# Optimization experiments

Measured on AMD Instinct MI355X. Metric: run time of the kernel, lower is better.

Reference implementation:

```python
import jax, jax.numpy as jnp
import numpy as np

N = 10000        # nodes
F_IN = 128       # node features (data.num_node_features)
OUT = 16         # out_channels
H = 32           # attention heads
C1 = 4 * OUT     # hidden per-head dim (4*out_channels)
E = 80000        # directed edges
EPS = 1e-5       # BatchNorm eps
NEG = 0.2        # GATConv LeakyReLU negative_slope


def _gat(x, src, dst, W, a_s, a_d, b, n, C):
    # PyG GATConv, shared lin, concat=False (mean over heads)
    h = (x @ W).reshape(n, H, C)                    # [n,H,C]
    e_src = jnp.sum(h * a_s, -1)                    # [n,H] (alpha from x_j)
    e_dst = jnp.sum(h * a_d, -1)                    # [n,H] (alpha from x_i)
    e = jax.nn.leaky_relu(e_src[src] + e_dst[dst], NEG)     # [E',H]
    m = jax.ops.segment_max(e, dst, num_segments=n)         # segment softmax
    p = jnp.exp(e - m[dst])
    z = jax.ops.segment_sum(p, dst, num_segments=n)
    alpha = p / z[dst]
    out = jax.ops.segment_sum(alpha[:, :, None] * h[src], dst, num_segments=n)
    return out.mean(1) + b                          # mean over heads + bias


def _bn(x, g, b, m, v):  # eval-mode BatchNorm1d (running stats)
    return (x - m) * g / jnp.sqrt(v + EPS) + b


def setup_inputs():
    k = jax.random.split(jax.random.key(0), 40)
    rn = lambda i, s, sc=0.1: jax.random.normal(k[i], s, jnp.float32) * sc
    d = {"x": jax.random.normal(k[0], (N, F_IN), jnp.float32),
         "edge_index": jax.random.randint(k[1], (2, E), 0, N, jnp.int32)}
    # 4 GATConv layers
    d.update(W1=rn(2, (F_IN, H * C1)), as1=rn(3, (H, C1)), ad1=rn(4, (H, C1)), b1=rn(5, (C1,)))
    d.update(W2=rn(6, (C1, H * OUT)), as2=rn(7, (H, OUT)), ad2=rn(8, (H, OUT)), b2=rn(9, (OUT,)))
    d.update(W3=rn(10, (F_IN, H * C1)), as3=rn(11, (H, C1)), ad3=rn(12, (H, C1)), b3=rn(13, (C1,)))
    d.update(W4=rn(14, (C1, H * OUT)), as4=rn(15, (H, OUT)), ad4=rn(16, (H, OUT)), b4=rn(17, (OUT,)))
    # ResidualNetwork(1 block): 1x1 Conv1d over L=1 == matmul
    d.update(rwa=rn(18, (F_IN, OUT)), rba=rn(19, (OUT,)),
             bn1g=jnp.ones(OUT), bn1b=jnp.zeros(OUT), bn1m=rn(20, (OUT,)), bn1v=jnp.abs(rn(21, (OUT,))) + 1.0,
             rwb=rn(22, (OUT, OUT)), rbb=rn(23, (OUT,)),
             bn2g=jnp.ones(OUT), bn2b=jnp.zeros(OUT), bn2m=rn(24, (OUT,)), bn2v=jnp.abs(rn(25, (OUT,))) + 1.0,
             wsc=rn(26, (F_IN, OUT)), bsc=rn(27, (OUT,)),
             bnsg=jnp.ones(OUT), bnsb=jnp.zeros(OUT), bnsm=rn(28, (OUT,)), bnsv=jnp.abs(rn(29, (OUT,))) + 1.0,
             wfc=rn(30, (OUT, OUT)), bfc=rn(31, (OUT,)))
    return d


def reference(x, edge_index, W1, as1, ad1, b1, W2, as2, ad2, b2,
              W3, as3, ad3, b3, W4, as4, ad4, b4,
              rwa, rba, bn1g, bn1b, bn1m, bn1v, rwb, rbb, bn2g, bn2b, bn2m, bn2v,
              wsc, bsc, bnsg, bnsb, bnsm, bnsv, wfc, bfc):
    n = x.shape[0]
    loops = jnp.arange(n, dtype=edge_index.dtype)  # add_self_loops=True
    s2t_src = jnp.concatenate([edge_index[0], loops])  # flow source_to_target
    s2t_dst = jnp.concatenate([edge_index[1], loops])
    t2s_src = jnp.concatenate([edge_index[1], loops])  # flow target_to_source
    t2s_dst = jnp.concatenate([edge_index[0], loops])
    # dropout in original is unassigned (no-op); eval mode assumed
    x_s = jax.nn.elu(_gat(x, s2t_src, s2t_dst, W1, as1, ad1, b1, n, C1))
    x_in = jax.nn.elu(_gat(x_s, s2t_src, s2t_dst, W2, as2, ad2, b2, n, OUT))
    x_t = jax.nn.elu(_gat(x, t2s_src, t2s_dst, W3, as3, ad3, b3, n, C1))
    x_out = jax.nn.elu(_gat(x_t, t2s_src, t2s_dst, W4, as4, ad4, b4, n, OUT))
    # ResidualNetwork: block + identity avg-pool (L=1) + fc
    h = jax.nn.relu(_bn(x @ rwa + rba, bn1g, bn1b, bn1m, bn1v))
    h = _bn(h @ rwb + rbb, bn2g, bn2b, bn2m, bn2v)
    sc = _bn(x @ wsc + bsc, bnsg, bnsb, bnsm, bnsv)
    x_self = jax.nn.relu(h + sc) @ wfc + bfc
    return (x_in, x_out, x_self)
```

## Files before the change

kernel.cpp:

```cpp
#include <hip/hip_runtime.h>
#include <stdint.h>

__device__ __forceinline__ float bf2f(unsigned short u) {
  union { unsigned int i; float f; } v; v.i = ((unsigned int)u) << 16; return v.f;
}
__device__ __forceinline__ unsigned short f2bf(float f) {
  union { float f; unsigned int i; } v; v.f = f;
  unsigned int i = v.i;
  unsigned int r = (i + 0x7fffu + ((i >> 16) & 1u)) >> 16;
  return (unsigned short)r;
}

typedef __bf16 bf16x8 __attribute__((ext_vector_type(8)));
typedef float f32x4 __attribute__((ext_vector_type(4)));
union ABfrag { int4 i4; bf16x8 v; };

#if __has_builtin(__builtin_amdgcn_cvt_pk_fp8_f32) && __has_builtin(__builtin_amdgcn_cvt_pk_f32_fp8)
#define HW_FP8 1
#else
#define HW_FP8 0
#endif

__device__ __forceinline__ unsigned char f2fp8_sw(float f) {
  union { float f; unsigned int u; } v; v.f = f;
  unsigned int s = (v.u >> 24) & 0x80;
  float a = fabsf(f);
  if (a >= 448.f) return (unsigned char)(s | 0x7E);
  v.f = a;
  int ex = (int)(v.u >> 23);
  unsigned int man = v.u & 0x7FFFFFu;
  if (ex >= 121) {
    unsigned int val = ((unsigned int)(ex - 120) << 3) | (man >> 20);
    unsigned int rem = man & 0xFFFFFu;
    if (rem > 0x80000u || (rem == 0x80000u && (val & 1))) val++;
    if (val > 0x7E) val = 0x7E;
    return (unsigned char)(s | val);
  }
  int q = (int)(a * 512.f + 0.5f);
  if (q > 8) q = 8;
  return (unsigned char)(s | (unsigned int)q);
}
__device__ __forceinline__ float fp8dec_sw(unsigned char c) {
  unsigned int e = (c >> 3) & 15u, m = c & 7u;
  float v;
  if (e) { union { unsigned int u; float f; } x; x.u = ((e + 120) << 23) | (m << 20); v = x.f; }
  else v = (float)m * 0.001953125f;
  return (c & 0x80) ? -v : v;
}
__device__ __forceinline__ unsigned char f2fp8(float f) {
#if HW_FP8
  int v = __builtin_amdgcn_cvt_pk_fp8_f32(f, f, 0, false);
  return (unsigned char)(v & 0xFF);
#else
  return f2fp8_sw(f);
#endif
}
__device__ __forceinline__ void dec16(int4 g, float o[16]) {
#if HW_FP8
  { auto p = __builtin_amdgcn_cvt_pk_f32_fp8(g.x, false); o[0]=p[0]; o[1]=p[1]; }
  { auto p = __builtin_amdgcn_cvt_pk_f32_fp8(g.x, true ); o[2]=p[0]; o[3]=p[1]; }
  { auto p = __builtin_amdgcn_cvt_pk_f32_fp8(g.y, false); o[4]=p[0]; o[5]=p[1]; }
  { auto p = __builtin_amdgcn_cvt_pk_f32_fp8(g.y, true ); o[6]=p[0]; o[7]=p[1]; }
  { auto p = __builtin_amdgcn_cvt_pk_f32_fp8(g.z, false); o[8]=p[0]; o[9]=p[1]; }
  { auto p = __builtin_amdgcn_cvt_pk_f32_fp8(g.z, true ); o[10]=p[0]; o[11]=p[1]; }
  { auto p = __builtin_amdgcn_cvt_pk_f32_fp8(g.w, false); o[12]=p[0]; o[13]=p[1]; }
  { auto p = __builtin_amdgcn_cvt_pk_f32_fp8(g.w, true ); o[14]=p[0]; o[15]=p[1]; }
#else
  unsigned int w[4] = {(unsigned)g.x, (unsigned)g.y, (unsigned)g.z, (unsigned)g.w};
#pragma unroll
  for (int d = 0; d < 4; ++d)
#pragma unroll
    for (int b = 0; b < 4; ++b) o[d*4+b] = fp8dec_sw((unsigned char)((w[d] >> (b*8)) & 0xFF));
#endif
}

__global__ __launch_bounds__(256) void k_detect(const unsigned int* __restrict__ x, int* flag) {
  __shared__ int cnt;
  if (threadIdx.x == 0) cnt = 0;
  __syncthreads();
  int c = 0;
  for (int i = threadIdx.x; i < 1024; i += 256) {
    unsigned int lo = x[i] & 0xFFFFu;
    int ex = (int)((lo >> 7) & 0xFF);
    if (ex >= 100 && ex <= 140) c++;
  }
  atomicAdd(&cnt, c);
  __syncthreads();
  if (threadIdx.x == 0) flag[0] = (cnt > 600) ? 1 : 0;
}

struct PrepDesc {
  const void* csrc[32]; float* cdst[32]; int cn[32];
  const void* x; float* xc; unsigned short* xp;
  const void* W1; const void* W2; const void* W3; const void* W4;
  unsigned short* P1; unsigned short* P2; unsigned short* P3; unsigned short* P4;
  int* degAB;
  int nxb;
  int xtotal;
  int ctotal;
  int ndeg2;
};
__global__ __launch_bounds__(256) void k_prep(PrepDesc d, const int* __restrict__ flag) {
  int isbf = *flag;
  int b = blockIdx.x;
  if (b < d.nxb) {
    int i = b * 256 + threadIdx.x;
    if (i < d.xtotal) {
      float v = isbf ? bf2f(((const unsigned short*)d.x)[i]) : ((const float*)d.x)[i];
      d.xc[i] = v;
      int row = i >> 7, c = i & 127;
      int tm = row >> 4, mr = row & 15;
      int s = c >> 5, quad = (c >> 3) & 3, j = c & 7;
      size_t idx = (((size_t)tm * 4 + s) * 64 + quad * 16 + mr) * 8 + j;
      d.xp[idx] = f2bf(v);
    }
    return;
  }
  b -= d.nxb;
  if (b < 288) {
    int u = b * 256 + threadIdx.x;
    const void* W; unsigned short* P; int K, N, lu;
    if (u < 32768)      { W = d.W1; P = d.P1; K = 128; N = 2048; lu = u; }
    else if (u < 36864) { W = d.W2; P = d.P2; K = 64;  N = 512;  lu = u - 32768; }
    else if (u < 69632) { W = d.W3; P = d.P3; K = 128; N = 2048; lu = u - 36864; }
    else                { W = d.W4; P = d.P4; K = 64;  N = 512;  lu = u - 69632; }
    int ksteps = K >> 5;
    int g = lu / (ksteps * 64);
    int rem = lu - g * (ksteps * 64);
    int s = rem >> 6, lane = rem & 63;
    int mr = lane & 15, quad = lane >> 4;
    int col = g * 16 + mr;
    int kbase = s * 32 + quad * 8;
#pragma unroll
    for (int j = 0; j < 8; ++j) {
      size_t src = (size_t)(kbase + j) * N + col;
      float v = isbf ? bf2f(((const unsigned short*)W)[src]) : ((const float*)W)[src];
      P[(size_t)lu * 8 + j] = f2bf(v);
    }
    return;
  }
  b -= 288;
  if (b < 4) {
    for (int idx = b * 256 + threadIdx.x; idx < d.ctotal; idx += 4 * 256) {
      int t = 0, off = idx;
      while (off >= d.cn[t]) { off -= d.cn[t]; ++t; }
      float v = isbf ? bf2f(((const unsigned short*)d.csrc[t])[off])
                     : ((const float*)d.csrc[t])[off];
      d.cdst[t][off] = v;
    }
    return;
  }
  b -= 4;
  for (int idx = b * 256 + threadIdx.x; idx < d.ndeg2; idx += 8 * 256) d.degAB[idx] = 0;
}

__global__ __launch_bounds__(256) void k_deg_count(const int* __restrict__ ei, int* degA, int* degB, int E) {
  int e = blockIdx.x * 256 + threadIdx.x;
  if (e < E) { atomicAdd(&degA[ei[E + e]], 1); atomicAdd(&degB[ei[e]], 1); }
}
__global__ __launch_bounds__(1024) void k_exscan2(const int* __restrict__ degA, const int* __restrict__ degB,
                                                  int* __restrict__ rowA, int* __restrict__ rowB,
                                                  int* __restrict__ colA, int* __restrict__ colB,
                                                  int* __restrict__ curA, int* __restrict__ curB, int n) {
  const int* deg = (blockIdx.x == 0) ? degA : degB;
  int* row = (blockIdx.x == 0) ? rowA : rowB;
  int* colx = (blockIdx.x == 0) ? colA : colB;
  int* curx = (blockIdx.x == 0) ? curA : curB;
  __shared__ int wsum[16], wbase[16];
  __shared__ int carry;
  if (threadIdx.x == 0) carry = 0;
  __syncthreads();
  int lane = threadIdx.x & 63, w = threadIdx.x >> 6;
  int chunks = (n + 1023) >> 10;
  for (int ch = 0; ch < chunks; ++ch) {
    int i = (ch << 10) + threadIdx.x;
    int v = (i < n) ? deg[i] : 0;
    int sc = v;
#pragma unroll
    for (int o = 1; o < 64; o <<= 1) { int t = __shfl_up(sc, o); if (lane >= o) sc += t; }
    if (lane == 63) wsum[w] = sc;
    __syncthreads();
    if (threadIdx.x < 16) {
      int v2 = wsum[threadIdx.x], s2 = v2;
#pragma unroll
      for (int o = 1; o < 16; o <<= 1) { int t = __shfl_up(s2, o); if (lane >= o) s2 += t; }
      wbase[threadIdx.x] = s2 - v2;
      if (threadIdx.x == 15) wsum[15] = s2;
    }
    __syncthreads();
    if (i < n) {
      int rv = carry + wbase[w] + (sc - v) + i;
      row[i] = rv;
      colx[rv] = i;
      curx[i] = rv + 1;
    }
    __syncthreads();
    if (threadIdx.x == 0) carry += wsum[15];
    __syncthreads();
  }
  if (threadIdx.x == 0) row[n] = carry + n;
}
__global__ __launch_bounds__(256) void k_scatter(const int* __restrict__ ei, int* colA, int* colB,
                                                 int* curA, int* curB, int E) {
  int e = blockIdx.x * 256 + threadIdx.x;
  if (e < E) {
    int s = ei[e], d = ei[E + e];
    colA[atomicAdd(&curA[d], 1)] = s;
    colB[atomicAdd(&curB[s], 1)] = d;
  }
}

template<int CH, int KSTEPS>
__global__ __launch_bounds__(256) void k_mm_es(const unsigned short* __restrict__ Ap,
                                               const unsigned short* __restrict__ Bp,
                                               unsigned char* __restrict__ C,
                                               const float* __restrict__ a_s,
                                               const float* __restrict__ a_d,
                                               float* __restrict__ es, float* __restrict__ ed,
                                               int M, int N) {
  __shared__ unsigned char tile[4][16][64];
  int wid = threadIdx.x >> 6;
  int wg = blockIdx.x * 4 + wid;
  int ntiles = N >> 6;
  int tm = wg / ntiles, tn = wg % ntiles;
  int lane = threadIdx.x & 63;
  int mr = lane & 15, quad = lane >> 4;
  const unsigned short* ap = Ap + ((size_t)tm * KSTEPS) * 512 + lane * 8;
  const unsigned short* bp = Bp + ((size_t)tn * 4 * KSTEPS) * 512 + lane * 8;
  f32x4 acc[4];
#pragma unroll
  for (int i = 0; i < 4; i++) acc[i] = (f32x4){0.f, 0.f, 0.f, 0.f};
#pragma unroll
  for (int s = 0; s < KSTEPS; ++s) {
    ABfrag a; a.i4 = *(const int4*)(ap + s * 512);
#pragma unroll
    for (int nt = 0; nt < 4; ++nt) {
      ABfrag b; b.i4 = *(const int4*)(bp + (size_t)(nt * KSTEPS + s) * 512);
      acc[nt] = __builtin_amdgcn_mfma_f32_16x16x32_bf16(a.v, b.v, acc[nt], 0, 0, 0);
    }
  }
#pragma unroll
  for (int nt = 0; nt < 4; ++nt)
#pragma unroll
    for (int r = 0; r < 4; ++r)
      tile[wid][quad * 4 + r][nt * 16 + mr] = f2fp8(acc[nt][r]);
  __syncthreads();
  {
    int r16 = lane >> 2, seg = lane & 3;
    int4 val = *(const int4*)&tile[wid][r16][seg * 16];
    *(int4*)(C + (size_t)(tm * 16 + r16) * N + tn * 64 + seg * 16) = val;
  }
  if (CH == 64) {
    float pes[4] = {0.f,0.f,0.f,0.f}, ped[4] = {0.f,0.f,0.f,0.f};
    const float* asr = a_s + tn * 64;
    const float* adr = a_d + tn * 64;
#pragma unroll
    for (int nt = 0; nt < 4; ++nt) {
      float ws = asr[nt * 16 + mr], wd = adr[nt * 16 + mr];
#pragma unroll
      for (int r = 0; r < 4; ++r) { pes[r] += acc[nt][r] * ws; ped[r] += acc[nt][r] * wd; }
    }
#pragma unroll
    for (int m = 1; m < 16; m <<= 1)
#pragma unroll
      for (int r = 0; r < 4; ++r) {
        pes[r] += __shfl_xor(pes[r], m);
        ped[r] += __shfl_xor(ped[r], m);
      }
    if (mr == 0) {
#pragma unroll
      for (int r = 0; r < 4; ++r) {
        int row = tm * 16 + quad * 4 + r;
        es[row * 32 + tn] = pes[r];
        ed[row * 32 + tn] = ped[r];
      }
    }
  } else {
    float pes[4][4], ped[4][4];
#pragma unroll
    for (int nt = 0; nt < 4; ++nt) {
      float ws = a_s[(tn * 4 + nt) * 16 + mr];
      float wd = a_d[(tn * 4 + nt) * 16 + mr];
#pragma unroll
      for (int r = 0; r < 4; ++r) { pes[nt][r] = acc[nt][r] * ws; ped[nt][r] = acc[nt][r] * wd; }
    }
#pragma unroll
    for (int m = 1; m < 16; m <<= 1)
#pragma unroll
      for (int nt = 0; nt < 4; ++nt)
#pragma unroll
        for (int r = 0; r < 4; ++r) {
          pes[nt][r] += __shfl_xor(pes[nt][r], m);
          ped[nt][r] += __shfl_xor(ped[nt][r], m);
        }
    if (mr == 0) {
#pragma unroll
      for (int nt = 0; nt < 4; ++nt)
#pragma unroll
        for (int r = 0; r < 4; ++r) {
          int row = tm * 16 + quad * 4 + r;
          es[row * 32 + tn * 4 + nt] = pes[nt][r];
          ed[row * 32 + tn * 4 + nt] = ped[nt][r];
        }
    }
  }
}

__device__ __forceinline__ float lrelu_clamp(float e) {
  e = (e > 0.f) ? e : 0.2f * e;
  return fminf(e, 80.f);
}

__global__ __launch_bounds__(256) void k_gather64(const unsigned char* __restrict__ h,
                                                  const float* __restrict__ es, const float* __restrict__ ed,
                                                  const int* __restrict__ rowp, const int* __restrict__ col,
                                                  const float* __restrict__ bias,
                                                  unsigned short* __restrict__ outp, int n) {
  int wid = threadIdx.x >> 6, lane = threadIdx.x & 63;
  int i = blockIdx.x * 4 + wid;
  if (i >= n) return;
  int hd0 = lane >> 2, hd1 = 16 + hd0;
  float e0 = ed[i * 32 + hd0];
  float e1 = ed[i * 32 + hd1];
  int beg = rowp[i], end = rowp[i + 1];
  int deg = end - beg;
  int colv = (lane < deg) ? col[beg + lane] : 0;
  float acc0[16], acc1[16];
#pragma unroll
  for (int k = 0; k < 16; ++k) { acc0[k] = 0.f; acc1[k] = 0.f; }
  float Z0 = 0.f, Z1 = 0.f;
  for (int j = 0; j < deg; ++j) {
    int s = (j < 64) ? __shfl(colv, j) : col[beg + j];
    const int4* hp = (const int4*)(h + (size_t)s * 2048);
    int4 g0 = hp[lane];
    int4 g1 = hp[64 + lane];
    float q0 = __expf(lrelu_clamp(es[s * 32 + hd0] + e0));
    float q1 = __expf(lrelu_clamp(es[s * 32 + hd1] + e1));
    Z0 += q0; Z1 += q1;
    float d0[16], d1[16];
    dec16(g0, d0); dec16(g1, d1);
#pragma unroll
    for (int k = 0; k < 16; ++k) { acc0[k] += q0 * d0[k]; acc1[k] += q1 * d1[k]; }
  }
  float zi0 = 1.0f / Z0, zi1 = 1.0f / Z1;
  float v[16];
#pragma unroll
  for (int k = 0; k < 16; ++k) v[k] = acc0[k] * zi0 + acc1[k] * zi1;
#pragma unroll
  for (int m = 4; m < 64; m <<= 1)
#pragma unroll
    for (int k = 0; k < 16; ++k) v[k] += __shfl_xor(v[k], m);
  if (lane < 4) {
    int tm = i >> 4, mr = i & 15;
    unsigned short ob[16];
#pragma unroll
    for (int k = 0; k < 16; ++k) {
      float t = v[k] * (1.f / 32.f) + bias[lane * 16 + k];
      t = (t > 0.f) ? t : (__expf(t) - 1.f);
      ob[k] = f2bf(t);
    }
    int s0 = lane >> 1;
#pragma unroll
    for (int g2 = 0; g2 < 2; ++g2) {
      size_t idx = (((size_t)tm * 2 + s0) * 64 + ((lane & 1) * 2 + g2) * 16 + mr) * 8;
      *(int4*)(outp + idx) = *(const int4*)(ob + g2 * 8);
    }
  }
}

__global__ __launch_bounds__(256) void k_gather16(const unsigned char* __restrict__ h,
                                                  const float* __restrict__ es, const float* __restrict__ ed,
                                                  const int* __restrict__ rowp, const int* __restrict__ col,
                                                  const float* __restrict__ bias,
                                                  void* __restrict__ outbase, size_t elem_off, int n,
                                                  const int* __restrict__ flag) {
  int wid = threadIdx.x >> 6, lane = threadIdx.x & 63;
  int i = blockIdx.x * 4 + wid;
  if (i >= n) return;
  int hh = lane & 31, j2 = lane >> 5;
  float ev = ed[i * 32 + hh];
  int beg = rowp[i], end = rowp[i + 1];
  int deg = end - beg;
  int colv = (lane < deg) ? col[beg + lane] : 0;
  float acc[16];
#pragma unroll
  for (int k = 0; k < 16; ++k) acc[k] = 0.f;
  float Z = 0.f;
  for (int j = j2; j < deg; j += 2) {
    int s = (j < 64) ? __shfl(colv, j) : col[beg + j];
    int4 g = ((const int4*)(h + (size_t)s * 512))[hh];
    float q = __expf(lrelu_clamp(es[s * 32 + hh] + ev));
    Z += q;
    float d[16];
    dec16(g, d);
#pragma unroll
    for (int k = 0; k < 16; ++k) acc[k] += q * d[k];
  }
  Z += __shfl_xor(Z, 32);
  float zi = 1.0f / Z;
  float v[16];
#pragma unroll
  for (int k = 0; k < 16; ++k) v[k] = acc[k] * zi;
#pragma unroll
  for (int m = 1; m < 64; m <<= 1)
#pragma unroll
    for (int k = 0; k < 16; ++k) v[k] += __shfl_xor(v[k], m);
  if (lane == 0) {
    int isbf = *flag;
    if (isbf) {
      unsigned short ob[16];
#pragma unroll
      for (int k = 0; k < 16; ++k) {
        float t = v[k] * (1.f / 32.f) + bias[k];
        t = (t > 0.f) ? t : (__expf(t) - 1.f);
        ob[k] = f2bf(t);
      }
      unsigned short* o = (unsigned short*)outbase + elem_off + (size_t)i * 16;
      *(int4*)o = *(const int4*)ob;
      *(int4*)(o + 8) = *(const int4*)(ob + 8);
    } else {
      float* o = (float*)outbase + elem_off + (size_t)i * 16;
#pragma unroll
      for (int k = 0; k < 16; ++k) {
        float t = v[k] * (1.f / 32.f) + bias[k];
        t = (t > 0.f) ? t : (__expf(t) - 1.f);
        o[k] = t;
      }
    }
  }
}

__global__ __launch_bounds__(256) void k_residual(const float* __restrict__ x,
    const float* __restrict__ rwa, const float* __restrict__ rba,
    const float* __restrict__ bn1g, const float* __restrict__ bn1b,
    const float* __restrict__ bn1m, const float* __restrict__ bn1v,
    const float* __restrict__ rwb, const float* __restrict__ rbb,
    const float* __restrict__ bn2g, const float* __restrict__ bn2b,
    const float* __restrict__ bn2m, const float* __restrict__ bn2v,
    const float* __restrict__ wsc, const float* __restrict__ bsc,
    const float* __restrict__ bnsg, const float* __restrict__ bnsb,
    const float* __restrict__ bnsm, const float* __restrict__ bnsv,
    const float* __restrict__ wfc, const float* __restrict__ bfc,
    void* __restrict__ outbase, size_t elem_off, int n, const int* __restrict__ flag) {
  __shared__ float xs[16][128];
  __shared__ float ha[16][16];
  __shared__ float tt[16][16];
  int nodebase = blockIdx.x * 16;
  for (int t = threadIdx.x; t < 16 * 128; t += 256)
    xs[t >> 7][t & 127] = x[(size_t)(nodebase + (t >> 7)) * 128 + (t & 127)];
  __syncthreads();
  int ni = threadIdx.x >> 4, c = threadIdx.x & 15;
  float ya = 0.f, ysc = 0.f;
  for (int k = 0; k < 128; ++k) {
    float xv = xs[ni][k];
    ya  += xv * rwa[k * 16 + c];
    ysc += xv * wsc[k * 16 + c];
  }
  ya += rba[c]; ysc += bsc[c];
  float s1 = bn1g[c] * rsqrtf(bn1v[c] + 1e-5f);
  ya = (ya - bn1m[c]) * s1 + bn1b[c];
  ya = fmaxf(ya, 0.f);
  float ss = bnsg[c] * rsqrtf(bnsv[c] + 1e-5f);
  ysc = (ysc - bnsm[c]) * ss + bnsb[c];
  ha[ni][c] = ya;
  __syncthreads();
  float h2 = rbb[c];
  for (int k = 0; k < 16; ++k) h2 += ha[ni][k] * rwb[k * 16 + c];
  float s2 = bn2g[c] * rsqrtf(bn2v[c] + 1e-5f);
  h2 = (h2 - bn2m[c]) * s2 + bn2b[c];
  tt[ni][c] = fmaxf(h2 + ysc, 0.f);
  __syncthreads();
  float o = bfc[c];
  for (int k = 0; k < 16; ++k) o += tt[ni][k] * wfc[k * 16 + c];
  size_t oo = elem_off + (size_t)(nodebase + ni) * 16 + c;
  if (*flag) ((unsigned short*)outbase)[oo] = f2bf(o);
  else       ((float*)outbase)[oo] = o;
}

extern "C" void kernel_launch(void* const* d_in, const int* in_sizes, int n_in,
                              void* d_out, int out_size, void* d_ws, size_t ws_size,
                              hipStream_t stream) {
  const int n = in_sizes[0] / 128;
  const int E = in_sizes[1] / 2;
  const int* ei = (const int*)d_in[1];

  char* wsp = (char*)d_ws; size_t off = 0;
  auto alloc = [&](size_t bytes) -> void* {
    void* p = wsp + off; off = (off + bytes + 255) & ~(size_t)255; return p;
  };
  int* flag = (int*)alloc(4);
  float* xc = (float*)alloc((size_t)n * 128 * 4);
  unsigned short* xp = (unsigned short*)alloc((size_t)n * 128 * 2);
  unsigned short* W1p = (unsigned short*)alloc((size_t)2048 * 128 * 2);
  unsigned short* W2p = (unsigned short*)alloc((size_t)512 * 64 * 2);
  unsigned short* W3p = (unsigned short*)alloc((size_t)2048 * 128 * 2);
  unsigned short* W4p = (unsigned short*)alloc((size_t)512 * 64 * 2);
  unsigned char* hbuf = (unsigned char*)alloc((size_t)n * 2048);
  unsigned char* hbuf2 = hbuf;
  float* es = (float*)alloc((size_t)n * 32 * 4);
  float* ed = (float*)alloc((size_t)n * 32 * 4);
  unsigned short* xsp = (unsigned short*)alloc((size_t)n * 64 * 2);
  unsigned short* xtp = (unsigned short*)alloc((size_t)n * 64 * 2);
  int* rowA = (int*)alloc((size_t)(n + 1) * 4);
  int* rowB = (int*)alloc((size_t)(n + 1) * 4);
  int* colA = (int*)alloc((size_t)(E + n) * 4);
  int* colB = (int*)alloc((size_t)(E + n) * 4);
  int* degAB = (int*)alloc((size_t)2 * n * 4);
  int* degA = degAB, * degB = degAB + n;
  int* curA = (int*)alloc((size_t)n * 4);
  int* curB = (int*)alloc((size_t)n * 4);

  static const int cidx[32] = {3,4,5, 7,8,9, 11,12,13, 15,16,17,
                               18,19,20,21,22,23,24,25,26,27,28,29,
                               30,31,32,33,34,35,36,37};
  PrepDesc pd;
  float* canon[38] = {nullptr};
  pd.ctotal = 0;
  for (int t = 0; t < 32; ++t) {
    int ii = cidx[t];
    canon[ii] = (float*)alloc((size_t)in_sizes[ii] * 4);
    pd.csrc[t] = d_in[ii];
    pd.cdst[t] = canon[ii];
    pd.cn[t] = in_sizes[ii];
    pd.ctotal += in_sizes[ii];
  }
  pd.x = d_in[0]; pd.xc = xc; pd.xp = xp;
  pd.W1 = d_in[2]; pd.W2 = d_in[6]; pd.W3 = d_in[10]; pd.W4 = d_in[14];
  pd.P1 = W1p; pd.P2 = W2p; pd.P3 = W3p; pd.P4 = W4p;
  pd.degAB = degAB;
  pd.nxb = (n * 128 + 255) / 256;
  pd.xtotal = n * 128;
  pd.ndeg2 = 2 * n;
  (void)ws_size; (void)n_in; (void)out_size;

  k_detect<<<1, 256, 0, stream>>>((const unsigned int*)d_in[0], flag);
  k_prep<<<pd.nxb + 288 + 4 + 8, 256, 0, stream>>>(pd, flag);

  k_deg_count<<<(E + 255) / 256, 256, 0, stream>>>(ei, degA, degB, E);
  k_exscan2<<<2, 1024, 0, stream>>>(degA, degB, rowA, rowB, colA, colB, curA, curB, n);
  k_scatter<<<(E + 255) / 256, 256, 0, stream>>>(ei, colA, colB, curA, curB, E);

  const int mt = n / 16;
  const int gb = (n + 3) / 4;
  k_mm_es<64,4><<<mt * 32 / 4, 256, 0, stream>>>(xp, W1p, hbuf, canon[3], canon[4], es, ed, n, 2048);
  k_gather64<<<gb, 256, 0, stream>>>(hbuf, es, ed, rowA, colA, canon[5], xsp, n);
  k_mm_es<16,2><<<mt * 8 / 4, 256, 0, stream>>>(xsp, W2p, hbuf2, canon[7], canon[8], es, ed, n, 512);
  k_gather16<<<gb, 256, 0, stream>>>(hbuf2, es, ed, rowA, colA, canon[9], d_out, 0, n, flag);
  k_mm_es<64,4><<<mt * 32 / 4, 256, 0, stream>>>(xp, W3p, hbuf, canon[11], canon[12], es, ed, n, 2048);
  k_gather64<<<gb, 256, 0, stream>>>(hbuf, es, ed, rowB, colB, canon[13], xtp, n);
  k_mm_es<16,2><<<mt * 8 / 4, 256, 0, stream>>>(xtp, W4p, hbuf2, canon[15], canon[16], es, ed, n, 512);
  k_gather16<<<gb, 256, 0, stream>>>(hbuf2, es, ed, rowB, colB, canon[17], d_out, (size_t)n * 16, n, flag);
  k_residual<<<n / 16, 256, 0, stream>>>(xc,
      canon[18], canon[19], canon[20], canon[21], canon[22], canon[23],
      canon[24], canon[25], canon[26], canon[27], canon[28], canon[29],
      canon[30], canon[31], canon[32], canon[33], canon[34], canon[35],
      canon[36], canon[37],
      d_out, (size_t)2 * n * 16, n, flag);
}
```

Before: 355.4 us.

## Batch the two GAT branches into shared launches and fold residual into first matmul

Runs the source-to-target and target-to-source GAT branches side by side. Each stage (the layer-1/3 matmul, the 64-channel gather, the layer-2/4 matmul, the 16-channel gather) becomes one launch over a doubled grid, and the residual network runs as extra blocks of the first matmul kernel. This cuts the kernel count from nine to four and gives each launch more blocks to fill the GPU, removing launch gaps and tail underutilization. In exchange the branches need separate h, es and ed buffers, which adds workspace and memory footprint.

```diff
diff --git a/kernel.cpp b/kernel.cpp
--- a/kernel.cpp
+++ b/kernel.cpp
@@ -74,6 +74,11 @@
 #endif
 }
 
+__device__ __forceinline__ float lrelu_clamp(float e) {
+  e = (e > 0.f) ? e : 0.2f * e;
+  return fminf(e, 80.f);
+}
+
 __global__ __launch_bounds__(256) void k_detect(const unsigned int* __restrict__ x, int* flag) {
   __shared__ int cnt;
   if (threadIdx.x == 0) cnt = 0;
@@ -95,10 +100,7 @@
   const void* W1; const void* W2; const void* W3; const void* W4;
   unsigned short* P1; unsigned short* P2; unsigned short* P3; unsigned short* P4;
   int* degAB;
-  int nxb;
-  int xtotal;
-  int ctotal;
-  int ndeg2;
+  int nxb, xtotal, ctotal, ndeg2;
 };
 __global__ __launch_bounds__(256) void k_prep(PrepDesc d, const int* __restrict__ flag) {
   int isbf = *flag;
@@ -210,17 +212,18 @@
   }
 }
 
+union SMem {
+  unsigned char tile[4][16][64];
+  struct { float xs[16][128]; float ha[16][16]; float tt[16][16]; } res;
+};
+
 template<int CH, int KSTEPS>
-__global__ __launch_bounds__(256) void k_mm_es(const unsigned short* __restrict__ Ap,
-                                               const unsigned short* __restrict__ Bp,
-                                               unsigned char* __restrict__ C,
-                                               const float* __restrict__ a_s,
-                                               const float* __restrict__ a_d,
-                                               float* __restrict__ es, float* __restrict__ ed,
-                                               int M, int N) {
-  __shared__ unsigned char tile[4][16][64];
+__device__ __forceinline__ void mm_es_body(int vblk,
+    const unsigned short* __restrict__ Ap, const unsigned short* __restrict__ Bp,
+    unsigned char* __restrict__ C, const float* __restrict__ a_s, const float* __restrict__ a_d,
+    float* __restrict__ es, float* __restrict__ ed, int N, SMem* sm) {
   int wid = threadIdx.x >> 6;
-  int wg = blockIdx.x * 4 + wid;
+  int wg = vblk * 4 + wid;
   int ntiles = N >> 6;
   int tm = wg / ntiles, tn = wg % ntiles;
   int lane = threadIdx.x & 63;
@@ -243,11 +246,11 @@
   for (int nt = 0; nt < 4; ++nt)
 #pragma unroll
     for (int r = 0; r < 4; ++r)
-      tile[wid][quad * 4 + r][nt * 16 + mr] = f2fp8(acc[nt][r]);
+      sm->tile[wid][quad * 4 + r][nt * 16 + mr] = f2fp8(acc[nt][r]);
   __syncthreads();
   {
     int r16 = lane >> 2, seg = lane & 3;
-    int4 val = *(const int4*)&tile[wid][r16][seg * 16];
+    int4 val = *(const int4*)&sm->tile[wid][r16][seg * 16];
     *(int4*)(C + (size_t)(tm * 16 + r16) * N + tn * 64 + seg * 16) = val;
   }
   if (CH == 64) {
@@ -306,18 +309,88 @@
   }
 }
 
-__device__ __forceinline__ float lrelu_clamp(float e) {
-  e = (e > 0.f) ? e : 0.2f * e;
-  return fminf(e, 80.f);
-}
-
-__global__ __launch_bounds__(256) void k_gather64(const unsigned char* __restrict__ h,
-                                                  const float* __restrict__ es, const float* __restrict__ ed,
-                                                  const int* __restrict__ rowp, const int* __restrict__ col,
-                                                  const float* __restrict__ bias,
-                                                  unsigned short* __restrict__ outp, int n) {
+struct MM13Desc {
+  const unsigned short* Ap;
+  const unsigned short* B1; const unsigned short* B3;
+  unsigned char* C1; unsigned char* C3;
+  const float* as1; const float* ad1; const float* as3; const float* ad3;
+  float* es1; float* ed1; float* es3; float* ed3;
+  int mmblks;
+  const float* xc;
+  const float* rp[20];
+  void* outbase; size_t eoff; int n;
+  const int* flag;
+};
+__global__ __launch_bounds__(256) void k_mm13res(MM13Desc d) {
+  __shared__ SMem sm;
+  int b = blockIdx.x;
+  if (b < d.mmblks) {
+    mm_es_body<64,4>(b, d.Ap, d.B1, d.C1, d.as1, d.ad1, d.es1, d.ed1, 2048, &sm);
+    return;
+  }
+  b -= d.mmblks;
+  if (b < d.mmblks) {
+    mm_es_body<64,4>(b, d.Ap, d.B3, d.C3, d.as3, d.ad3, d.es3, d.ed3, 2048, &sm);
+    return;
+  }
+  b -= d.mmblks;
+  int nodebase = b * 16;
+  for (int t = threadIdx.x; t < 16 * 128; t += 256)
+    sm.res.xs[t >> 7][t & 127] = d.xc[(size_t)(nodebase + (t >> 7)) * 128 + (t & 127)];
+  __syncthreads();
+  int ni = threadIdx.x >> 4, c = threadIdx.x & 15;
+  const float* rwa = d.rp[0]; const float* rba = d.rp[1];
+  const float* bn1g = d.rp[2]; const float* bn1b = d.rp[3];
+  const float* bn1m = d.rp[4]; const float* bn1v = d.rp[5];
+  const float* rwb = d.rp[6]; const float* rbb = d.rp[7];
+  const float* bn2g = d.rp[8]; const float* bn2b = d.rp[9];
+  const float* bn2m = d.rp[10]; const float* bn2v = d.rp[11];
+  const float* wsc = d.rp[12]; const float* bsc = d.rp[13];
+  const float* bnsg = d.rp[14]; const float* bnsb = d.rp[15];
+  const float* bnsm = d.rp[16]; const float* bnsv = d.rp[17];
+  const float* wfc = d.rp[18]; const float* bfc = d.rp[19];
+  float ya = 0.f, ysc = 0.f;
+  for (int k = 0; k < 128; ++k) {
+    float xv = sm.res.xs[ni][k];
+    ya  += xv * rwa[k * 16 + c];
+    ysc += xv * wsc[k * 16 + c];
+  }
+  ya += rba[c]; ysc += bsc[c];
+  float s1 = bn1g[c] * rsqrtf(bn1v[c] + 1e-5f);
+  ya = (ya - bn1m[c]) * s1 + bn1b[c];
+  ya = fmaxf(ya, 0.f);
+  float ss = bnsg[c] * rsqrtf(bnsv[c] + 1e-5f);
+  ysc = (ysc - bnsm[c]) * ss + bnsb[c];
+  sm.res.ha[ni][c] = ya;
+  __syncthreads();
+  float h2 = rbb[c];
+  for (int k = 0; k < 16; ++k) h2 += sm.res.ha[ni][k] * rwb[k * 16 + c];
+  float s2 = bn2g[c] * rsqrtf(bn2v[c] + 1e-5f);
+  h2 = (h2 - bn2m[c]) * s2 + bn2b[c];
+  sm.res.tt[ni][c] = fmaxf(h2 + ysc, 0.f);
+  __syncthreads();
+  float o = bfc[c];
+  for (int k = 0; k < 16; ++k) o += sm.res.tt[ni][k] * wfc[k * 16 + c];
+  size_t oo = d.eoff + (size_t)(nodebase + ni) * 16 + c;
+  if (*d.flag) ((unsigned short*)d.outbase)[oo] = f2bf(o);
+  else         ((float*)d.outbase)[oo] = o;
+}
+
+__global__ __launch_bounds__(256) void k_g64(const unsigned char* __restrict__ h1,
+                                             const unsigned char* __restrict__ h3,
+                                             const float* __restrict__ es1, const float* __restrict__ ed1,
+                                             const float* __restrict__ es3, const float* __restrict__ ed3,
+                                             const int* __restrict__ rowA, const int* __restrict__ colA,
+                                             const int* __restrict__ rowB, const int* __restrict__ colB,
+                                             const float* __restrict__ b1, const float* __restrict__ b3,
+                                             unsigned short* __restrict__ xsp, unsigned short* __restrict__ xtp,
+                                             int n, int gb) {
+  int b = blockIdx.x;
+  const unsigned char* h; const float *es, *ed, *bias; const int *rowp, *col; unsigned short* outp;
+  if (b < gb) { h = h1; es = es1; ed = ed1; rowp = rowA; col = colA; bias = b1; outp = xsp; }
+  else { b -= gb; h = h3; es = es3; ed = ed3; rowp = rowB; col = colB; bias = b3; outp = xtp; }
   int wid = threadIdx.x >> 6, lane = threadIdx.x & 63;
-  int i = blockIdx.x * 4 + wid;
+  int i = b * 4 + wid;
   if (i >= n) return;
   int hd0 = lane >> 2, hd1 = 16 + hd0;
   float e0 = ed[i * 32 + hd0];
@@ -368,14 +441,39 @@
   }
 }
 
-__global__ __launch_bounds__(256) void k_gather16(const unsigned char* __restrict__ h,
-                                                  const float* __restrict__ es, const float* __restrict__ ed,
-                                                  const int* __restrict__ rowp, const int* __restrict__ col,
-                                                  const float* __restrict__ bias,
-                                                  void* __restrict__ outbase, size_t elem_off, int n,
-                                                  const int* __restrict__ flag) {
+__global__ __launch_bounds__(256) void k_mm24(const unsigned short* __restrict__ xsp,
+                                              const unsigned short* __restrict__ xtp,
+                                              const unsigned short* __restrict__ W2p,
+                                              const unsigned short* __restrict__ W4p,
+                                              unsigned char* __restrict__ h2, unsigned char* __restrict__ h4,
+                                              const float* __restrict__ as2, const float* __restrict__ ad2,
+                                              const float* __restrict__ as4, const float* __restrict__ ad4,
+                                              float* __restrict__ es2, float* __restrict__ ed2,
+                                              float* __restrict__ es4, float* __restrict__ ed4,
+                                              int mmblks) {
+  __shared__ SMem sm;
+  int b = blockIdx.x;
+  if (b < mmblks)
+    mm_es_body<16,2>(b, xsp, W2p, h2, as2, ad2, es2, ed2, 512, &sm);
+  else
+    mm_es_body<16,2>(b - mmblks, xtp, W4p, h4, as4, ad4, es4, ed4, 512, &sm);
+}
+
+__global__ __launch_bounds__(256) void k_g16(const unsigned char* __restrict__ h2,
+                                             const unsigned char* __restrict__ h4,
+                                             const float* __restrict__ es2, const float* __restrict__ ed2,
+                                             const float* __restrict__ es4, const float* __restrict__ ed4,
+                                             const int* __restrict__ rowA, const int* __restrict__ colA,
+                                             const int* __restrict__ rowB, const int* __restrict__ colB,
+                                             const float* __restrict__ b2, const float* __restrict__ b4,
+                                             void* __restrict__ outbase, int n, int gb,
+                                             const int* __restrict__ flag) {
+  int b = blockIdx.x;
+  const unsigned char* h; const float *es, *ed, *bias; const int *rowp, *col; size_t eoff;
+  if (b < gb) { h = h2; es = es2; ed = ed2; rowp = rowA; col = colA; bias = b2; eoff = 0; }
+  else { b -= gb; h = h4; es = es4; ed = ed4; rowp = rowB; col = colB; bias = b4; eoff = (size_t)n * 16; }
   int wid = threadIdx.x >> 6, lane = threadIdx.x & 63;
-  int i = blockIdx.x * 4 + wid;
+  int i = b * 4 + wid;
   if (i >= n) return;
   int hh = lane & 31, j2 = lane >> 5;
   float ev = ed[i * 32 + hh];
@@ -415,11 +513,11 @@
         t = (t > 0.f) ? t : (__expf(t) - 1.f);
         ob[k] = f2bf(t);
       }
-      unsigned short* o = (unsigned short*)outbase + elem_off + (size_t)i * 16;
+      unsigned short* o = (unsigned short*)outbase + eoff + (size_t)i * 16;
       *(int4*)o = *(const int4*)ob;
       *(int4*)(o + 8) = *(const int4*)(ob + 8);
     } else {
-      float* o = (float*)outbase + elem_off + (size_t)i * 16;
+      float* o = (float*)outbase + eoff + (size_t)i * 16;
 #pragma unroll
       for (int k = 0; k < 16; ++k) {
         float t = v[k] * (1.f / 32.f) + bias[k];
@@ -428,53 +526,6 @@
       }
     }
   }
-}
-
-__global__ __launch_bounds__(256) void k_residual(const float* __restrict__ x,
-    const float* __restrict__ rwa, const float* __restrict__ rba,
-    const float* __restrict__ bn1g, const float* __restrict__ bn1b,
-    const float* __restrict__ bn1m, const float* __restrict__ bn1v,
-    const float* __restrict__ rwb, const float* __restrict__ rbb,
-    const float* __restrict__ bn2g, const float* __restrict__ bn2b,
-    const float* __restrict__ bn2m, const float* __restrict__ bn2v,
-    const float* __restrict__ wsc, const float* __restrict__ bsc,
-    const float* __restrict__ bnsg, const float* __restrict__ bnsb,
-    const float* __restrict__ bnsm, const float* __restrict__ bnsv,
-    const float* __restrict__ wfc, const float* __restrict__ bfc,
-    void* __restrict__ outbase, size_t elem_off, int n, const int* __restrict__ flag) {
-  __shared__ float xs[16][128];
-  __shared__ float ha[16][16];
-  __shared__ float tt[16][16];
-  int nodebase = blockIdx.x * 16;
-  for (int t = threadIdx.x; t < 16 * 128; t += 256)
-    xs[t >> 7][t & 127] = x[(size_t)(nodebase + (t >> 7)) * 128 + (t & 127)];
-  __syncthreads();
-  int ni = threadIdx.x >> 4, c = threadIdx.x & 15;
-  float ya = 0.f, ysc = 0.f;
-  for (int k = 0; k < 128; ++k) {
-    float xv = xs[ni][k];
-    ya  += xv * rwa[k * 16 + c];
-    ysc += xv * wsc[k * 16 + c];
-  }
-  ya += rba[c]; ysc += bsc[c];
-  float s1 = bn1g[c] * rsqrtf(bn1v[c] + 1e-5f);
-  ya = (ya - bn1m[c]) * s1 + bn1b[c];
-  ya = fmaxf(ya, 0.f);
-  float ss = bnsg[c] * rsqrtf(bnsv[c] + 1e-5f);
-  ysc = (ysc - bnsm[c]) * ss + bnsb[c];
-  ha[ni][c] = ya;
-  __syncthreads();
-  float h2 = rbb[c];
-  for (int k = 0; k < 16; ++k) h2 += ha[ni][k] * rwb[k * 16 + c];
-  float s2 = bn2g[c] * rsqrtf(bn2v[c] + 1e-5f);
-  h2 = (h2 - bn2m[c]) * s2 + bn2b[c];
-  tt[ni][c] = fmaxf(h2 + ysc, 0.f);
-  __syncthreads();
-  float o = bfc[c];
-  for (int k = 0; k < 16; ++k) o += tt[ni][k] * wfc[k * 16 + c];
-  size_t oo = elem_off + (size_t)(nodebase + ni) * 16 + c;
-  if (*flag) ((unsigned short*)outbase)[oo] = f2bf(o);
-  else       ((float*)outbase)[oo] = o;
 }
 
 extern "C" void kernel_launch(void* const* d_in, const int* in_sizes, int n_in,
@@ -495,10 +546,18 @@
   unsigned short* W2p = (unsigned short*)alloc((size_t)512 * 64 * 2);
   unsigned short* W3p = (unsigned short*)alloc((size_t)2048 * 128 * 2);
   unsigned short* W4p = (unsigned short*)alloc((size_t)512 * 64 * 2);
-  unsigned char* hbuf = (unsigned char*)alloc((size_t)n * 2048);
-  unsigned char* hbuf2 = hbuf;
-  float* es = (float*)alloc((size_t)n * 32 * 4);
-  float* ed = (float*)alloc((size_t)n * 32 * 4);
+  unsigned char* h1 = (unsigned char*)alloc((size_t)n * 2048);
+  unsigned char* h3 = (unsigned char*)alloc((size_t)n * 2048);
+  unsigned char* h2 = (unsigned char*)alloc((size_t)n * 512);
+  unsigned char* h4 = (unsigned char*)alloc((size_t)n * 512);
+  float* es1 = (float*)alloc((size_t)n * 32 * 4);
+  float* ed1 = (float*)alloc((size_t)n * 32 * 4);
+  float* es3 = (float*)alloc((size_t)n * 32 * 4);
+  float* ed3 = (float*)alloc((size_t)n * 32 * 4);
+  float* es2 = (float*)alloc((size_t)n * 32 * 4);
+  float* ed2 = (float*)alloc((size_t)n * 32 * 4);
+  float* es4 = (float*)alloc((size_t)n * 32 * 4);
+  float* ed4 = (float*)alloc((size_t)n * 32 * 4);
   unsigned short* xsp = (unsigned short*)alloc((size_t)n * 64 * 2);
   unsigned short* xtp = (unsigned short*)alloc((size_t)n * 64 * 2);
   int* rowA = (int*)alloc((size_t)(n + 1) * 4);
@@ -541,19 +600,27 @@
   k_scatter<<<(E + 255) / 256, 256, 0, stream>>>(ei, colA, colB, curA, curB, E);
 
   const int mt = n / 16;
+  const int mmblks64 = mt * 32 / 4;
+  const int mmblks16 = mt * 8 / 4;
   const int gb = (n + 3) / 4;
-  k_mm_es<64,4><<<mt * 32 / 4, 256, 0, stream>>>(xp, W1p, hbuf, canon[3], canon[4], es, ed, n, 2048);
-  k_gather64<<<gb, 256, 0, stream>>>(hbuf, es, ed, rowA, colA, canon[5], xsp, n);
-  k_mm_es<16,2><<<mt * 8 / 4, 256, 0, stream>>>(xsp, W2p, hbuf2, canon[7], canon[8], es, ed, n, 512);
-  k_gather16<<<gb, 256, 0, stream>>>(hbuf2, es, ed, rowA, colA, canon[9], d_out, 0, n, flag);
-  k_mm_es<64,4><<<mt * 32 / 4, 256, 0, stream>>>(xp, W3p, hbuf, canon[11], canon[12], es, ed, n, 2048);
-  k_gather64<<<gb, 256, 0, stream>>>(hbuf, es, ed, rowB, colB, canon[13], xtp, n);
-  k_mm_es<16,2><<<mt * 8 / 4, 256, 0, stream>>>(xtp, W4p, hbuf2, canon[15], canon[16], es, ed, n, 512);
-  k_gather16<<<gb, 256, 0, stream>>>(hbuf2, es, ed, rowB, colB, canon[17], d_out, (size_t)n * 16, n, flag);
-  k_residual<<<n / 16, 256, 0, stream>>>(xc,
-      canon[18], canon[19], canon[20], canon[21], canon[22], canon[23],
-      canon[24], canon[25], canon[26], canon[27], canon[28], canon[29],
-      canon[30], canon[31], canon[32], canon[33], canon[34], canon[35],
-      canon[36], canon[37],
-      d_out, (size_t)2 * n * 16, n, flag);
-}
+
+  MM13Desc md;
+  md.Ap = xp; md.B1 = W1p; md.B3 = W3p; md.C1 = h1; md.C3 = h3;
+  md.as1 = canon[3]; md.ad1 = canon[4]; md.as3 = canon[11]; md.ad3 = canon[12];
+  md.es1 = es1; md.ed1 = ed1; md.es3 = es3; md.ed3 = ed3;
+  md.mmblks = mmblks64;
+  md.xc = xc;
+  for (int t = 0; t < 20; ++t) md.rp[t] = canon[18 + t];
+  md.outbase = d_out; md.eoff = (size_t)2 * n * 16; md.n = n; md.flag = flag;
+  k_mm13res<<<2 * mmblks64 + n / 16, 256, 0, stream>>>(md);
+
+  k_g64<<<2 * gb, 256, 0, stream>>>(h1, h3, es1, ed1, es3, ed3,
+                                    rowA, colA, rowB, colB,
+                                    canon[5], canon[13], xsp, xtp, n, gb);
+  k_mm24<<<2 * mmblks16, 256, 0, stream>>>(xsp, xtp, W2p, W4p, h2, h4,
+                                           canon[7], canon[8], canon[15], canon[16],
+                                           es2, ed2, es4, ed4, mmblks16);
+  k_g16<<<2 * gb, 256, 0, stream>>>(h2, h4, es2, ed2, es4, ed4,
+                                    rowA, colA, rowB, colB,
+                                    canon[9], canon[17], d_out, n, gb, flag);
+}
```

Measured after the change: 323.8 us. 8.9% less time.
